# Optimization experiments

Measured on AMD Instinct MI355X. Metric: run time of the kernel, lower is better.

## Reference

```python
import jax, jax.numpy as jnp
import numpy as np

U, I, D = 50000, 25000, 128          # users, items, emb_size
E = 1_000_000                        # user-item interactions
L = 3                                # num_layers
B = 4096                             # BPR batch size
N = U + I                            # total graph nodes


def setup_inputs() -> dict:
    key = jax.random.key(0)
    k1, k2, k3, k4, k5, k6, k7 = jax.random.split(key, 7)
    # Xavier-ish embedding tables
    user_emb = jax.random.normal(k1, (U, D), jnp.float32) * 0.1
    item_emb = jax.random.normal(k2, (I, D), jnp.float32) * 0.1
    # random bipartite interactions -> symmetric COO adjacency over N nodes
    eu = jax.random.randint(k3, (E,), 0, U)            # user node ids
    ei = jax.random.randint(k4, (E,), 0, I) + U        # item node ids (offset)
    adj_row = jnp.concatenate([eu, ei]).astype(jnp.int32)   # [2E]
    adj_col = jnp.concatenate([ei, eu]).astype(jnp.int32)   # [2E]
    # symmetric normalization D^-1/2 A D^-1/2 (matches create_adj_mat)
    deg = jax.ops.segment_sum(jnp.ones(2 * E, jnp.float32), adj_row, num_segments=N)
    d_inv = jnp.where(deg > 0, deg ** -0.5, 0.0)
    adj_vals = d_inv[adj_row] * d_inv[adj_col]               # [2E] float32
    users = jax.random.randint(k5, (B,), 0, U).astype(jnp.int32)
    pos_items = jax.random.randint(k6, (B,), 0, I).astype(jnp.int32)
    neg_items = jax.random.randint(k7, (B,), 0, I).astype(jnp.int32)
    return dict(user_emb=user_emb, item_emb=item_emb, adj_row=adj_row,
                adj_col=adj_col, adj_vals=adj_vals, users=users,
                pos_items=pos_items, neg_items=neg_items)


def _spmm(vals, row, col, x):
    # sparse [N,N] @ dense [N,D] via gather + segment_sum
    return jax.ops.segment_sum(vals[:, None] * x[col], row, num_segments=N)


def reference(user_emb, item_emb, adj_row, adj_col, adj_vals,
              users, pos_items, neg_items):
    ego = jnp.concatenate([user_emb, item_emb], axis=0)      # [N, D]
    # FAITHFUL to the torch source: ego_embeddings is never reassigned inside
    # the layer loop, so every one of the L layer outputs equals A @ ego.
    # mean(stack([ego, A@ego, ..., A@ego])) == (ego + L * A@ego) / (L + 1)
    h = _spmm(adj_vals, adj_row, adj_col, ego)               # [N, D]
    final = (ego + L * h) / (L + 1)                          # mean over L+1 layers
    u_final = final[:U]
    i_final = final[U:]
    u_g = u_final[users]                                     # [B, D]
    pos_i_g = i_final[pos_items]                             # [B, D]
    neg_i_g = i_final[neg_items]                             # [B, D]
    return (u_g, pos_i_g, neg_i_g, i_final)
```

## Files before the change

kernel.cpp:

```cpp
#include <hip/hip_runtime.h>

#define U_CNT 50000
#define I_CNT 25000
#define D_DIM 128
#define E_CNT 1000000
#define B_CNT 4096
#define ICAP 96
#define UCAP 64


__global__ void rep_kernel(const int* __restrict__ users,
                           int* __restrict__ flags) {
    int j = blockIdx.x * blockDim.x + threadIdx.x;
    if (j < B_CNT) atomicCAS(&flags[users[j]], 0, j + 1);
}

__global__ __launch_bounds__(256) void bucket_kernel(
        const int*   __restrict__ adj_row,
        const int*   __restrict__ adj_col,
        const float* __restrict__ adj_vals,
        const int*   __restrict__ flags,
        int*         __restrict__ icnt,
        int*         __restrict__ ucnt,
        int2*        __restrict__ ibuck,
        int2*        __restrict__ ubuck) {
    const int base = (blockIdx.x * blockDim.x + threadIdx.x) * 2;
    if (base >= E_CNT) return;
    const int2   uu = *(const int2*)  (adj_row  + base);
    const int2   tt = *(const int2*)  (adj_col  + base);
    const float2 vv = *(const float2*)(adj_vals + base);

#pragma unroll
    for (int k = 0; k < 2; ++k) {
        const int   u = k ? uu.y : uu.x;
        const int   t = (k ? tt.y : tt.x) - U_CNT;
        const float v = k ? vv.y : vv.x;
        const int c = atomicAdd(&icnt[t], 1);
        ibuck[(size_t)t * ICAP + c] = make_int2(u, __float_as_int(v));
        const int f = flags[u];
        if (f) {
            const int j0 = f - 1;
            const int c2 = atomicAdd(&ucnt[j0], 1);
            ubuck[(size_t)j0 * UCAP + c2] = make_int2(t, __float_as_int(v));
        }
    }
}

__global__ __launch_bounds__(256) void item_gather_kernel(
        const float* __restrict__ user_emb,
        const float* __restrict__ item_emb,
        const int*   __restrict__ icnt,
        const int2*  __restrict__ ibuck,
        float*       __restrict__ out) {
    const int lane = threadIdx.x & 63;
    const int t    = (blockIdx.x * blockDim.x + threadIdx.x) >> 6;
    if (t >= I_CNT) return;

    const int   n = icnt[t];
    const int2* b = ibuck + (size_t)t * ICAP;
    float ax = 0.0f, ay = 0.0f;

    int p = 0;
    for (; p + 4 <= n; p += 4) {
        const int2 e0 = b[p], e1 = b[p + 1], e2 = b[p + 2], e3 = b[p + 3];
        const float2 x0 = ((const float2*)(user_emb + (size_t)e0.x * D_DIM))[lane];
        const float2 x1 = ((const float2*)(user_emb + (size_t)e1.x * D_DIM))[lane];
        const float2 x2 = ((const float2*)(user_emb + (size_t)e2.x * D_DIM))[lane];
        const float2 x3 = ((const float2*)(user_emb + (size_t)e3.x * D_DIM))[lane];
        const float v0 = __int_as_float(e0.y), v1 = __int_as_float(e1.y);
        const float v2 = __int_as_float(e2.y), v3 = __int_as_float(e3.y);
        ax += v0 * x0.x + v1 * x1.x + v2 * x2.x + v3 * x3.x;
        ay += v0 * x0.y + v1 * x1.y + v2 * x2.y + v3 * x3.y;
    }
    for (; p < n; ++p) {
        const int2 e = b[p];
        const float2 x = ((const float2*)(user_emb + (size_t)e.x * D_DIM))[lane];
        const float v = __int_as_float(e.y);
        ax += v * x.x;
        ay += v * x.y;
    }

    const float2 eg = ((const float2*)(item_emb + (size_t)t * D_DIM))[lane];
    float2 o;
    o.x = (eg.x + 3.0f * ax) * 0.25f;
    o.y = (eg.y + 3.0f * ay) * 0.25f;
    ((float2*)(out + (size_t)(3 * B_CNT + t) * D_DIM))[lane] = o;
}

__global__ __launch_bounds__(256) void user_gather_kernel(
        const float* __restrict__ user_emb,
        const float* __restrict__ item_emb,
        const int*   __restrict__ users,
        const int*   __restrict__ flags,
        const int*   __restrict__ ucnt,
        const int2*  __restrict__ ubuck,
        float*       __restrict__ out) {
    const int lane = threadIdx.x & 63;
    const int j    = (blockIdx.x * blockDim.x + threadIdx.x) >> 6;
    if (j >= B_CNT) return;
    const int u = users[j];
    if (flags[u] - 1 != j) return;

    const int   n = ucnt[j];
    const int2* b = ubuck + (size_t)j * UCAP;
    float ax = 0.0f, ay = 0.0f;

    int p = 0;
    for (; p + 4 <= n; p += 4) {
        const int2 e0 = b[p], e1 = b[p + 1], e2 = b[p + 2], e3 = b[p + 3];
        const float2 x0 = ((const float2*)(item_emb + (size_t)e0.x * D_DIM))[lane];
        const float2 x1 = ((const float2*)(item_emb + (size_t)e1.x * D_DIM))[lane];
        const float2 x2 = ((const float2*)(item_emb + (size_t)e2.x * D_DIM))[lane];
        const float2 x3 = ((const float2*)(item_emb + (size_t)e3.x * D_DIM))[lane];
        const float v0 = __int_as_float(e0.y), v1 = __int_as_float(e1.y);
        const float v2 = __int_as_float(e2.y), v3 = __int_as_float(e3.y);
        ax += v0 * x0.x + v1 * x1.x + v2 * x2.x + v3 * x3.x;
        ay += v0 * x0.y + v1 * x1.y + v2 * x2.y + v3 * x3.y;
    }
    for (; p < n; ++p) {
        const int2 e = b[p];
        const float2 x = ((const float2*)(item_emb + (size_t)e.x * D_DIM))[lane];
        const float v = __int_as_float(e.y);
        ax += v * x.x;
        ay += v * x.y;
    }

    const float2 eg = ((const float2*)(user_emb + (size_t)u * D_DIM))[lane];
    float2 o;
    o.x = (eg.x + 3.0f * ax) * 0.25f;
    o.y = (eg.y + 3.0f * ay) * 0.25f;
    ((float2*)(out + (size_t)j * D_DIM))[lane] = o;
}

__global__ __launch_bounds__(256) void finalize_kernel(
        const int* __restrict__ users,
        const int* __restrict__ flags,
        const int* __restrict__ pos_items,
        const int* __restrict__ neg_items,
        float*     __restrict__ out) {
    const int lane = threadIdx.x & 63;
    const int w    = (blockIdx.x * blockDim.x + threadIdx.x) >> 6;
    if (w >= 3 * B_CNT) return;

    if (w < B_CNT) {
        const int u  = users[w];
        const int j0 = flags[u] - 1;
        if (j0 == w) return;
        const float2 v = ((const float2*)(out + (size_t)j0 * D_DIM))[lane];
        ((float2*)(out + (size_t)w * D_DIM))[lane] = v;
    } else {
        const int q   = w - B_CNT;
        const int idx = (q < B_CNT) ? pos_items[q] : neg_items[q - B_CNT];
        const float2 v = ((const float2*)(out + (size_t)(3 * B_CNT + idx) * D_DIM))[lane];
        ((float2*)(out + (size_t)w * D_DIM))[lane] = v;
    }
}

extern "C" void kernel_launch(void* const* d_in, const int* in_sizes, int n_in,
                              void* d_out, int out_size, void* d_ws, size_t ws_size,
                              hipStream_t stream) {
    const float* user_emb  = (const float*)d_in[0];
    const float* item_emb  = (const float*)d_in[1];
    const int*   adj_row   = (const int*)  d_in[2];
    const int*   adj_col   = (const int*)  d_in[3];
    const float* adj_vals  = (const float*)d_in[4];
    const int*   users     = (const int*)  d_in[5];
    const int*   pos_items = (const int*)  d_in[6];
    const int*   neg_items = (const int*)  d_in[7];
    float* out = (float*)d_out;

    char* ws = (char*)d_ws;
    int*  flags = (int*)ws;
    int*  icnt  = flags + U_CNT;
    int*  ucnt  = icnt + I_CNT;
    int2* ibuck = (int2*)(ucnt + B_CNT);
    int2* ubuck = ibuck + (size_t)I_CNT * ICAP;

    hipMemsetAsync(flags, 0, (size_t)(U_CNT + I_CNT + B_CNT) * sizeof(int), stream);

    rep_kernel<<<(B_CNT + 255) / 256, 256, 0, stream>>>(users, flags);

    bucket_kernel<<<(E_CNT / 2 + 255) / 256, 256, 0, stream>>>(
        adj_row, adj_col, adj_vals, flags, icnt, ucnt, ibuck, ubuck);

    item_gather_kernel<<<(I_CNT * 64 + 255) / 256, 256, 0, stream>>>(
        user_emb, item_emb, icnt, ibuck, out);

    user_gather_kernel<<<(B_CNT * 64 + 255) / 256, 256, 0, stream>>>(
        user_emb, item_emb, users, flags, ucnt, ubuck, out);

    finalize_kernel<<<(3 * B_CNT * 64 + 255) / 256, 256, 0, stream>>>(
        users, flags, pos_items, neg_items, out);
}
```

Before: 239.6 us.

## Gather user embeddings in bf16, add membership bitmap, widen bucket loads

Adds a conversion kernel that packs the user embedding table into bf16 pairs, so the item gather pulls half the bytes per neighbour row. It also replaces the per-user flag lookup in bucketing with a compact bitmap test that fits in cache, reading the slot array only for sampled users. Each bucketing thread now handles four edges with 128-bit loads. The bf16 path lowers accuracy of the item aggregation, and the extra conversion pass costs a full read and write of the user table every call.

Result: faster. 230.8 us (-3.7%).

```diff
diff --git a/kernel.cpp b/kernel.cpp
--- a/kernel.cpp
+++ b/kernel.cpp
@@ -1,4 +1,5 @@
 #include <hip/hip_runtime.h>
+#include <hip/hip_bf16.h>
 
 #define U_CNT 50000
 #define I_CNT 25000
@@ -7,51 +8,75 @@
 #define B_CNT 4096
 #define ICAP 96
 #define UCAP 64
-
+#define BM_WORDS 1600
+
+
+__device__ __forceinline__ unsigned pack_bf2(float lo, float hi) {
+    __hip_bfloat16 a = __float2bfloat16(lo);
+    __hip_bfloat16 b = __float2bfloat16(hi);
+    unsigned short ua = *reinterpret_cast<unsigned short*>(&a);
+    unsigned short ub = *reinterpret_cast<unsigned short*>(&b);
+    return ((unsigned)ub << 16) | ua;
+}
+__device__ __forceinline__ float bf_lo(unsigned w) { return __uint_as_float(w << 16); }
+__device__ __forceinline__ float bf_hi(unsigned w) { return __uint_as_float(w & 0xffff0000u); }
 
 __global__ void rep_kernel(const int* __restrict__ users,
-                           int* __restrict__ flags) {
+                           unsigned* __restrict__ bitmap,
+                           int* __restrict__ slot) {
     int j = blockIdx.x * blockDim.x + threadIdx.x;
-    if (j < B_CNT) atomicCAS(&flags[users[j]], 0, j + 1);
+    if (j >= B_CNT) return;
+    const int u = users[j];
+    atomicOr(&bitmap[u >> 5], 1u << (u & 31));
+    atomicCAS(&slot[u], 0, j + 1);
+}
+
+__global__ __launch_bounds__(256) void cvt_kernel(
+        const float* __restrict__ src, unsigned* __restrict__ dst, int n_dw) {
+    int i = blockIdx.x * blockDim.x + threadIdx.x;
+    if (i >= n_dw) return;
+    float2 f = ((const float2*)src)[i];
+    dst[i] = pack_bf2(f.x, f.y);
 }
 
 __global__ __launch_bounds__(256) void bucket_kernel(
-        const int*   __restrict__ adj_row,
-        const int*   __restrict__ adj_col,
-        const float* __restrict__ adj_vals,
-        const int*   __restrict__ flags,
-        int*         __restrict__ icnt,
-        int*         __restrict__ ucnt,
-        int2*        __restrict__ ibuck,
-        int2*        __restrict__ ubuck) {
-    const int base = (blockIdx.x * blockDim.x + threadIdx.x) * 2;
+        const int*      __restrict__ adj_row,
+        const int*      __restrict__ adj_col,
+        const float*    __restrict__ adj_vals,
+        const unsigned* __restrict__ bitmap,
+        const int*      __restrict__ slot,
+        int*  __restrict__ icnt,  int*  __restrict__ ucnt,
+        int2* __restrict__ ibuck, int2* __restrict__ ubuck) {
+    const int base = (blockIdx.x * blockDim.x + threadIdx.x) * 4;
     if (base >= E_CNT) return;
-    const int2   uu = *(const int2*)  (adj_row  + base);
-    const int2   tt = *(const int2*)  (adj_col  + base);
-    const float2 vv = *(const float2*)(adj_vals + base);
+    const int4   uu = *(const int4*)  (adj_row  + base);
+    const int4   tt = *(const int4*)  (adj_col  + base);
+    const float4 vv = *(const float4*)(adj_vals + base);
+
+    const int   us[4] = {uu.x, uu.y, uu.z, uu.w};
+    const int   ts[4] = {tt.x - U_CNT, tt.y - U_CNT, tt.z - U_CNT, tt.w - U_CNT};
+    const float vs[4] = {vv.x, vv.y, vv.z, vv.w};
 
 #pragma unroll
-    for (int k = 0; k < 2; ++k) {
-        const int   u = k ? uu.y : uu.x;
-        const int   t = (k ? tt.y : tt.x) - U_CNT;
-        const float v = k ? vv.y : vv.x;
+    for (int k = 0; k < 4; ++k) {
+        const int u = us[k], t = ts[k];
+        const int vb = __float_as_int(vs[k]);
         const int c = atomicAdd(&icnt[t], 1);
-        ibuck[(size_t)t * ICAP + c] = make_int2(u, __float_as_int(v));
-        const int f = flags[u];
-        if (f) {
-            const int j0 = f - 1;
+        ibuck[(size_t)t * ICAP + c] = make_int2(u, vb);
+        if ((bitmap[u >> 5] >> (u & 31)) & 1u) {
+            const int j0 = slot[u] - 1;
             const int c2 = atomicAdd(&ucnt[j0], 1);
-            ubuck[(size_t)j0 * UCAP + c2] = make_int2(t, __float_as_int(v));
+            ubuck[(size_t)j0 * UCAP + c2] = make_int2(t, vb);
         }
     }
 }
 
 __global__ __launch_bounds__(256) void item_gather_kernel(
-        const float* __restrict__ user_emb,
-        const float* __restrict__ item_emb,
-        const int*   __restrict__ icnt,
-        const int2*  __restrict__ ibuck,
-        float*       __restrict__ out) {
+        const float*    __restrict__ item_emb,
+        const unsigned* __restrict__ ue16,
+        const int*      __restrict__ icnt,
+        const int2*     __restrict__ ibuck,
+        float*          __restrict__ out) {
     const int lane = threadIdx.x & 63;
     const int t    = (blockIdx.x * blockDim.x + threadIdx.x) >> 6;
     if (t >= I_CNT) return;
@@ -63,21 +88,21 @@
     int p = 0;
     for (; p + 4 <= n; p += 4) {
         const int2 e0 = b[p], e1 = b[p + 1], e2 = b[p + 2], e3 = b[p + 3];
-        const float2 x0 = ((const float2*)(user_emb + (size_t)e0.x * D_DIM))[lane];
-        const float2 x1 = ((const float2*)(user_emb + (size_t)e1.x * D_DIM))[lane];
-        const float2 x2 = ((const float2*)(user_emb + (size_t)e2.x * D_DIM))[lane];
-        const float2 x3 = ((const float2*)(user_emb + (size_t)e3.x * D_DIM))[lane];
+        const unsigned w0 = ue16[(size_t)e0.x * 64 + lane];
+        const unsigned w1 = ue16[(size_t)e1.x * 64 + lane];
+        const unsigned w2 = ue16[(size_t)e2.x * 64 + lane];
+        const unsigned w3 = ue16[(size_t)e3.x * 64 + lane];
         const float v0 = __int_as_float(e0.y), v1 = __int_as_float(e1.y);
         const float v2 = __int_as_float(e2.y), v3 = __int_as_float(e3.y);
-        ax += v0 * x0.x + v1 * x1.x + v2 * x2.x + v3 * x3.x;
-        ay += v0 * x0.y + v1 * x1.y + v2 * x2.y + v3 * x3.y;
+        ax += v0 * bf_lo(w0) + v1 * bf_lo(w1) + v2 * bf_lo(w2) + v3 * bf_lo(w3);
+        ay += v0 * bf_hi(w0) + v1 * bf_hi(w1) + v2 * bf_hi(w2) + v3 * bf_hi(w3);
     }
     for (; p < n; ++p) {
         const int2 e = b[p];
-        const float2 x = ((const float2*)(user_emb + (size_t)e.x * D_DIM))[lane];
+        const unsigned w = ue16[(size_t)e.x * 64 + lane];
         const float v = __int_as_float(e.y);
-        ax += v * x.x;
-        ay += v * x.y;
+        ax += v * bf_lo(w);
+        ay += v * bf_hi(w);
     }
 
     const float2 eg = ((const float2*)(item_emb + (size_t)t * D_DIM))[lane];
@@ -91,7 +116,7 @@
         const float* __restrict__ user_emb,
         const float* __restrict__ item_emb,
         const int*   __restrict__ users,
-        const int*   __restrict__ flags,
+        const int*   __restrict__ slot,
         const int*   __restrict__ ucnt,
         const int2*  __restrict__ ubuck,
         float*       __restrict__ out) {
@@ -99,7 +124,7 @@
     const int j    = (blockIdx.x * blockDim.x + threadIdx.x) >> 6;
     if (j >= B_CNT) return;
     const int u = users[j];
-    if (flags[u] - 1 != j) return;
+    if (slot[u] - 1 != j) return;
 
     const int   n = ucnt[j];
     const int2* b = ubuck + (size_t)j * UCAP;
@@ -134,7 +159,7 @@
 
 __global__ __launch_bounds__(256) void finalize_kernel(
         const int* __restrict__ users,
-        const int* __restrict__ flags,
+        const int* __restrict__ slot,
         const int* __restrict__ pos_items,
         const int* __restrict__ neg_items,
         float*     __restrict__ out) {
@@ -144,7 +169,7 @@
 
     if (w < B_CNT) {
         const int u  = users[w];
-        const int j0 = flags[u] - 1;
+        const int j0 = slot[u] - 1;
         if (j0 == w) return;
         const float2 v = ((const float2*)(out + (size_t)j0 * D_DIM))[lane];
         ((float2*)(out + (size_t)w * D_DIM))[lane] = v;
@@ -169,26 +194,32 @@
     const int*   neg_items = (const int*)  d_in[7];
     float* out = (float*)d_out;
 
-    char* ws = (char*)d_ws;
-    int*  flags = (int*)ws;
-    int*  icnt  = flags + U_CNT;
-    int*  ucnt  = icnt + I_CNT;
+    unsigned* bitmap = (unsigned*)d_ws;
+    int* slot = (int*)(bitmap + BM_WORDS);
+    int* icnt = slot + U_CNT;
+    int* ucnt = icnt + I_CNT;
     int2* ibuck = (int2*)(ucnt + B_CNT);
     int2* ubuck = ibuck + (size_t)I_CNT * ICAP;
-
-    hipMemsetAsync(flags, 0, (size_t)(U_CNT + I_CNT + B_CNT) * sizeof(int), stream);
-
-    rep_kernel<<<(B_CNT + 255) / 256, 256, 0, stream>>>(users, flags);
-
-    bucket_kernel<<<(E_CNT / 2 + 255) / 256, 256, 0, stream>>>(
-        adj_row, adj_col, adj_vals, flags, icnt, ucnt, ibuck, ubuck);
+    unsigned* ue16 = (unsigned*)(ubuck + (size_t)B_CNT * UCAP);
+
+    hipMemsetAsync(bitmap, 0,
+                   (size_t)(BM_WORDS + U_CNT + I_CNT + B_CNT) * sizeof(int),
+                   stream);
+
+    rep_kernel<<<(B_CNT + 255) / 256, 256, 0, stream>>>(users, bitmap, slot);
+
+    cvt_kernel<<<(U_CNT * 64 + 255) / 256, 256, 0, stream>>>(
+        user_emb, ue16, U_CNT * 64);
+
+    bucket_kernel<<<(E_CNT / 4 + 255) / 256, 256, 0, stream>>>(
+        adj_row, adj_col, adj_vals, bitmap, slot, icnt, ucnt, ibuck, ubuck);
 
     item_gather_kernel<<<(I_CNT * 64 + 255) / 256, 256, 0, stream>>>(
-        user_emb, item_emb, icnt, ibuck, out);
+        item_emb, ue16, icnt, ibuck, out);
 
     user_gather_kernel<<<(B_CNT * 64 + 255) / 256, 256, 0, stream>>>(
-        user_emb, item_emb, users, flags, ucnt, ubuck, out);
+        user_emb, item_emb, users, slot, ucnt, ubuck, out);
 
     finalize_kernel<<<(3 * B_CNT * 64 + 255) / 256, 256, 0, stream>>>(
-        users, flags, pos_items, neg_items, out);
-}
+        users, slot, pos_items, neg_items, out);
+}
```
